# Kernel tuning notes

Hardware: AMD Instinct MI355X
Metric: run time of the kernel (lower is better)

Reference implementation:

```python
import jax, jax.numpy as jnp
import numpy as np

B, S, D, H = 2, 2048, 1024, 16
HD = D // H                 # head_dim = 64
BLOCK = 16                  # _DEFAULT_BLOCK_SIZE
NB = S // BLOCK             # max_blocks_per_seq = 128
WINDOW = 512
NEG = jnp.float32(-1e30)


def setup_inputs() -> dict:
    key = jax.random.key(0)
    ks = jax.random.split(key, 5)
    x = jax.random.normal(ks[0], (B, S, D), jnp.float32)
    scale = D ** -0.5
    wq = jax.random.normal(ks[1], (D, D), jnp.float32) * scale
    wk = jax.random.normal(ks[2], (D, D), jnp.float32) * scale
    wv = jax.random.normal(ks[3], (D, D), jnp.float32) * scale
    wo = jax.random.normal(ks[4], (D, D), jnp.float32) * scale
    # sequential paged layout (matches the module's synthesized-cache fallback)
    block_tables = jnp.arange(B * NB, dtype=jnp.int32).reshape(B, NB)
    slot_mapping = jnp.arange(B * S, dtype=jnp.int32)
    context_lens = jnp.full((B,), S, dtype=jnp.int32)
    return {"x": x, "wq": wq, "wk": wk, "wv": wv, "wo": wo,
            "block_tables": block_tables, "slot_mapping": slot_mapping,
            "context_lens": context_lens, "window_size": WINDOW}


def reference(x, wq, wk, wv, wo, block_tables, slot_mapping, context_lens, window_size):
    b, s, d = x.shape
    # Q/K/V projections (nn.Linear, bias=False: y = x @ W^T)
    q = (x @ wq.T).reshape(b, s, H, HD)
    k = (x @ wk.T).reshape(b, s, H, HD)
    v = (x @ wv.T).reshape(b, s, H, HD)

    # ---- memopt_C.write_cache: scatter K/V into the physical slot pool ----
    num_slots = b * s
    key_cache = jnp.zeros((num_slots, H, HD), x.dtype).at[slot_mapping].set(k.reshape(-1, H, HD))
    value_cache = jnp.zeros((num_slots, H, HD), x.dtype).at[slot_mapping].set(v.reshape(-1, H, HD))

    # ---- dynamic_sparse_attention: read KV through block_tables ----
    t = jnp.arange(s)
    # physical slot of logical token t of sequence b: block_tables[b, t//BLOCK]*BLOCK + t%BLOCK
    slots = block_tables[:, t // BLOCK].astype(jnp.int32) * BLOCK + (t % BLOCK)[None, :].astype(jnp.int32)  # [B,S]
    kc = key_cache[slots]    # [B,S,H,HD]
    vc = value_cache[slots]  # [B,S,H,HD]

    scores = jnp.einsum('bqhd,bkhd->bhqk', q, kc) * (HD ** -0.5)  # [B,H,S,S]
    qpos = t[:, None]
    kpos = t[None, :]
    # causal + window-limited visibility (window_size tokens of history)
    vis = (kpos <= qpos) & (qpos - kpos < window_size)            # [S,S]
    ctx = t[None, :] < context_lens[:, None]                       # [B,S]
    mask = vis[None, None, :, :] & ctx[:, None, None, :]
    scores = jnp.where(mask, scores, NEG)
    attn = jax.nn.softmax(scores, axis=-1)
    out = jnp.einsum('bhqk,bkhd->bqhd', attn, vc).reshape(b, s, d)
    return out @ wo.T
```

## Files before the change

### kernel.cpp

```cpp
#include <hip/hip_runtime.h>

typedef __attribute__((ext_vector_type(4))) float  f32x4;
typedef __attribute__((ext_vector_type(8))) short  bf16x8;

typedef __attribute__((address_space(3))) void lds_void_t;
typedef __attribute__((address_space(1))) void g_void_t;

#define S_LEN  2048
#define DMODEL 1024
#define NHEAD  16
#define HDIM   64
#define NBLK   128
#define BATCH  2
#define KT     64
#define VP     72

__device__ __forceinline__ short f2bf(float f) {
  union { float f; unsigned u; } v; v.f = f;
  unsigned r = v.u + 0x7fffu + ((v.u >> 16) & 1u);
  return (short)(r >> 16);
}

__global__ __launch_bounds__(256) void cvt_all_kernel(
    const float* __restrict__ x,  const float* __restrict__ wq,
    const float* __restrict__ wk, const float* __restrict__ wv,
    const float* __restrict__ wo,
    short* __restrict__ xb,  short* __restrict__ wqb,
    short* __restrict__ wkb, short* __restrict__ wvb,
    short* __restrict__ wob) {
  const long i = ((long)blockIdx.x * 256 + threadIdx.x) * 8;
  const float* s; short* d; long off;
  if (i < 4194304L)      { s = x;  d = xb;  off = i; }
  else if (i < 5242880L) { s = wq; d = wqb; off = i - 4194304L; }
  else if (i < 6291456L) { s = wk; d = wkb; off = i - 5242880L; }
  else if (i < 7340032L) { s = wv; d = wvb; off = i - 6291456L; }
  else                   { s = wo; d = wob; off = i - 7340032L; }
  f32x4 a = *(const f32x4*)(s + off);
  f32x4 b = *(const f32x4*)(s + off + 4);
  bf16x8 o;
  o[0]=f2bf(a[0]); o[1]=f2bf(a[1]); o[2]=f2bf(a[2]); o[3]=f2bf(a[3]);
  o[4]=f2bf(b[0]); o[5]=f2bf(b[1]); o[6]=f2bf(b[2]); o[7]=f2bf(b[3]);
  *(bf16x8*)(d + off) = o;
}

__global__ __launch_bounds__(512, 2) void gemm8_kernel(
    const short* __restrict__ A,
    const short* __restrict__ W0, const short* __restrict__ W1, const short* __restrict__ W2,
    const int* __restrict__ slot_map,
    short* __restrict__ qbuf, short* __restrict__ kcache, short* __restrict__ vcache)
{
  extern __shared__ short smem[];

  const int bid0 = (int)blockIdx.y * 16 + (int)blockIdx.x;
  const int bid  = (bid0 & 7) * 32 + (bid0 >> 3);
  const int m0 = (bid & 15) * 256;
  const int n0 = (bid >> 4) * 192;
  const short* Ag = A + (size_t)m0 * DMODEL;

  const int tid  = threadIdx.x;
  const int wave = tid >> 6, lane = tid & 63;
  const int l15 = lane & 15, lg = lane >> 4;
  const int wr = wave >> 2, wc = wave & 3;
  const int swz = l15 & 7;

  f32x4 acc[8][3];
#pragma unroll
  for (int m = 0; m < 8; m++)
#pragma unroll
    for (int n = 0; n < 3; n++) acc[m][n] = (f32x4)0.f;

#define STG_A(BUFI, K0, P) {                                                               \
    const int g_ = (P) * 512 + tid;                                                        \
    const int r_ = g_ >> 3;                                                                \
    const int cs_ = (g_ & 7) ^ (r_ & 7);                                                   \
    __builtin_amdgcn_global_load_lds((g_void_t*)(Ag + (size_t)r_ * DMODEL + (K0) + cs_ * 8), \
        (lds_void_t*)(smem + (BUFI) * 16384 + ((P) * 512 + wave * 64) * 8), 16, 0, 0); }

#define STG_B(BUFI, K0, P) {                                                               \
    const int g_ = (P) * 512 + tid;                                                        \
    const int r_ = g_ >> 3;                                                                \
    const int grow = n0 + r_;                                                              \
    const short* wb = (grow < 1024) ? W0 : (grow < 2048) ? W1 : W2;                        \
    const int cs_ = (g_ & 7) ^ (r_ & 7);                                                   \
    __builtin_amdgcn_global_load_lds((g_void_t*)(wb + (size_t)(grow & 1023) * DMODEL + (K0) + cs_ * 8), \
        (lds_void_t*)(smem + 49152 + (BUFI) * 12288 + ((P) * 512 + wave * 64) * 8), 16, 0, 0); }

#define BAR() do { asm volatile("" ::: "memory");                \
    __builtin_amdgcn_s_barrier();                                \
    asm volatile("" ::: "memory"); } while (0)

#define LGKM0() asm volatile("s_waitcnt lgkmcnt(0)" ::: "memory")

#define RD_B(BUF)                                                                          \
    _Pragma("unroll") for (int nt = 0; nt < 3; ++nt) {                                     \
      const int row = wc * 48 + nt * 16 + l15;                                             \
      _Pragma("unroll") for (int ks = 0; ks < 2; ++ks)                                     \
        bfr[nt][ks] = *(const bf16x8*)((BUF) + row * 64 + (((ks * 4 + lg) ^ swz) << 3)); }

#define RD_A2(BUF, MQ)                                                                     \
    _Pragma("unroll") for (int mi = 0; mi < 2; ++mi) {                                     \
      const int row = wr * 128 + ((MQ) * 2 + mi) * 16 + l15;                               \
      _Pragma("unroll") for (int ks = 0; ks < 2; ++ks)                                     \
        af[mi][ks] = *(const bf16x8*)((BUF) + row * 64 + (((ks * 4 + lg) ^ swz) << 3)); }

#define MMA2(MQ)                                                                           \
    __builtin_amdgcn_s_setprio(1);                                                         \
    _Pragma("unroll") for (int mi = 0; mi < 2; ++mi)                                       \
    _Pragma("unroll") for (int nt = 0; nt < 3; ++nt)                                       \
    _Pragma("unroll") for (int ks = 0; ks < 2; ++ks)                                       \
      acc[(MQ) * 2 + mi][nt] = __builtin_amdgcn_mfma_f32_16x16x32_bf16(                    \
          af[mi][ks], bfr[nt][ks], acc[(MQ) * 2 + mi][nt], 0, 0, 0);                       \
    __builtin_amdgcn_s_setprio(0);

  const int NT = DMODEL / 64;

  STG_A(0, 0, 0); STG_A(0, 0, 1); STG_A(0, 0, 2); STG_A(0, 0, 3);
  STG_B(0, 0, 0); STG_B(0, 0, 1); STG_B(0, 0, 2);
  STG_A(1, 64, 0); STG_A(1, 64, 1); STG_A(1, 64, 2); STG_A(1, 64, 3);
  asm volatile("s_waitcnt vmcnt(4)" ::: "memory");
  BAR();

  for (int t = 0; t < NT; ++t) {
    const short* Ab = smem + (t % 3) * 16384;
    const short* Bb = smem + 49152 + (t & 1) * 12288;
    const int bB = (t + 1) & 1;
    const int bA = (t + 2) % 3;
    const int k1 = (t + 1) * 64;
    const int k2 = (t + 2) * 64;
    const bool sB = (t + 1 < NT);
    const bool sA = (t + 2 < NT);

    bf16x8 af[2][2], bfr[3][2];

    RD_B(Bb);
    RD_A2(Ab, 0);
    if (sB) { STG_B(bB, k1, 0); }
    if (sA) { STG_A(bA, k2, 0); }
    BAR(); LGKM0();
    MMA2(0);

    RD_A2(Ab, 1);
    if (sB) { STG_B(bB, k1, 1); }
    if (sA) { STG_A(bA, k2, 1); }
    BAR(); LGKM0();
    MMA2(1);

    RD_A2(Ab, 2);
    if (sB) { STG_B(bB, k1, 2); }
    if (sA) { STG_A(bA, k2, 2); }
    BAR(); LGKM0();
    MMA2(2);

    RD_A2(Ab, 3);
    if (sA) { STG_A(bA, k2, 3); }
    BAR(); LGKM0();
    MMA2(3);
    if (t < NT - 2)       { asm volatile("s_waitcnt vmcnt(2)" ::: "memory"); BAR(); }
    else if (t == NT - 2) { asm volatile("s_waitcnt vmcnt(0)" ::: "memory"); BAR(); }
  }
#undef STG_A
#undef STG_B
#undef BAR
#undef LGKM0
#undef RD_B
#undef RD_A2
#undef MMA2

#pragma unroll
  for (int mf = 0; mf < 8; ++mf) {
    const int rowb = m0 + wr * 128 + mf * 16 + lg * 4;
#pragma unroll
    for (int r4 = 0; r4 < 4; ++r4) {
      const int row = rowb + r4;
      const int slot = slot_map[row];
#pragma unroll
      for (int nt = 0; nt < 3; ++nt) {
        const int col = n0 + wc * 48 + nt * 16 + l15;
        const short bv = f2bf(acc[mf][nt][r4]);
        if (col < DMODEL)
          qbuf[(size_t)row * DMODEL + col] = bv;
        else if (col < 2 * DMODEL)
          kcache[(size_t)slot * DMODEL + (col - DMODEL)] = bv;
        else
          vcache[(size_t)slot * DMODEL + (col - 2 * DMODEL)] = bv;
      }
    }
  }
}

__global__ __launch_bounds__(256, 2) void gemm1_kernel(
    const short* __restrict__ A, const short* __restrict__ W,
    float* __restrict__ outf)
{
  extern __shared__ short smem1[];

  const int bid0 = (int)blockIdx.y * 32 + (int)blockIdx.x;
  const int bid  = (bid0 & 7) * 32 + (bid0 >> 3);
  const int m0 = (bid & 31) * 128;
  const int n0 = (bid >> 5) * 128;
  const short* Ag = A + (size_t)m0 * DMODEL;
  const short* Bg = W + (size_t)n0 * DMODEL;

  const int tid = threadIdx.x;
  const int wave = tid >> 6, lane = tid & 63;
  const int l15 = lane & 15, lg = lane >> 4;
  const int wr = wave >> 1, wc = wave & 1;
  const int swz = l15 & 7;

  short* const As0 = smem1;
  short* const Bs0 = smem1 + 8192;
  short* const As1 = smem1 + 16384;
  short* const Bs1 = smem1 + 24576;

  f32x4 acc[4][4];
#pragma unroll
  for (int m = 0; m < 4; m++)
#pragma unroll
    for (int n = 0; n < 4; n++) acc[m][n] = (f32x4)0.f;

#define STG1(LA, LB, K0) {                                                                 \
    _Pragma("unroll") for (int p = 0; p < 4; ++p) {                                        \
      const int u = p * 256 + tid; const int r = u >> 3; const int cs = (u & 7) ^ (r & 7); \
      __builtin_amdgcn_global_load_lds((g_void_t*)(Ag + (size_t)r * DMODEL + (K0) + cs * 8), \
          (lds_void_t*)((LA) + (p * 256 + wave * 64) * 8), 16, 0, 0); }                    \
    _Pragma("unroll") for (int p = 0; p < 4; ++p) {                                        \
      const int u = p * 256 + tid; const int r = u >> 3; const int cs = (u & 7) ^ (r & 7); \
      __builtin_amdgcn_global_load_lds((g_void_t*)(Bg + (size_t)r * DMODEL + (K0) + cs * 8), \
          (lds_void_t*)((LB) + (p * 256 + wave * 64) * 8), 16, 0, 0); } }

  STG1(As0, Bs0, 0);
  asm volatile("s_waitcnt vmcnt(0)" ::: "memory");
  __builtin_amdgcn_s_barrier();
  asm volatile("" ::: "memory");

  for (int t = 0; t < 16; ++t) {
    const int cur = t & 1;
    short* const Ac = cur ? As1 : As0;
    short* const Bc = cur ? Bs1 : Bs0;
    short* const An = cur ? As0 : As1;
    short* const Bn = cur ? Bs0 : Bs1;
    if (t + 1 < 16) {
      STG1(An, Bn, (t + 1) * 64);
      asm volatile("s_waitcnt vmcnt(8)" ::: "memory");
    } else {
      asm volatile("s_waitcnt vmcnt(0)" ::: "memory");
    }
    asm volatile("" ::: "memory");
    __builtin_amdgcn_s_barrier();
    asm volatile("" ::: "memory");

    bf16x8 af[4][2], bfr[4][2];
#pragma unroll
    for (int m4 = 0; m4 < 4; ++m4) {
      const int row = wr * 64 + m4 * 16 + l15;
#pragma unroll
      for (int ks = 0; ks < 2; ++ks)
        af[m4][ks] = *(const bf16x8*)(Ac + row * 64 + (((ks * 4 + lg) ^ swz) << 3));
    }
#pragma unroll
    for (int n4 = 0; n4 < 4; ++n4) {
      const int row = wc * 64 + n4 * 16 + l15;
#pragma unroll
      for (int ks = 0; ks < 2; ++ks)
        bfr[n4][ks] = *(const bf16x8*)(Bc + row * 64 + (((ks * 4 + lg) ^ swz) << 3));
    }
    __builtin_amdgcn_s_setprio(1);
#pragma unroll
    for (int m4 = 0; m4 < 4; ++m4)
#pragma unroll
      for (int n4 = 0; n4 < 4; ++n4)
#pragma unroll
        for (int ks = 0; ks < 2; ++ks)
          acc[m4][n4] = __builtin_amdgcn_mfma_f32_16x16x32_bf16(af[m4][ks], bfr[n4][ks], acc[m4][n4], 0, 0, 0);
    __builtin_amdgcn_s_setprio(0);

    asm volatile("" ::: "memory");
    __builtin_amdgcn_s_barrier();
    asm volatile("" ::: "memory");
  }
#undef STG1

#pragma unroll
  for (int m4 = 0; m4 < 4; ++m4) {
    const int rowb = m0 + wr * 64 + m4 * 16 + lg * 4;
#pragma unroll
    for (int n4 = 0; n4 < 4; ++n4) {
      const int col = n0 + wc * 64 + n4 * 16 + l15;
#pragma unroll
      for (int r4 = 0; r4 < 4; ++r4)
        outf[(size_t)(rowb + r4) * DMODEL + col] = acc[m4][n4][r4];
    }
  }
}

__global__ __launch_bounds__(512, 4) void attn_kernel(
    const short* __restrict__ qbuf,
    const short* __restrict__ kcache, const short* __restrict__ vcache,
    const int* __restrict__ block_tables, const int* __restrict__ context_lens,
    const int* __restrict__ window_size,
    short* __restrict__ attn_out)
{
  __shared__ short Ks[KT * 64];
  __shared__ short Vt[HDIM * VP];
  __shared__ short Pb[8 * 16 * VP];

  const int b = blockIdx.z, h = blockIdx.y;
  const int bx = (b & 1) ? ((int)gridDim.x - 1 - (int)blockIdx.x) : (int)blockIdx.x;
  const int q0 = bx * 128;
  const int ctx = context_lens[b];
  const int ws  = window_size[0];
  const int* bt = block_tables + b * NBLK;

  const int tid  = threadIdx.x;
  const int wave = tid >> 6, lane = tid & 63;
  const int l15 = lane & 15, lg = lane >> 4;
  const int qw = q0 + wave * 16;

  const short* qp = qbuf + ((size_t)(b * S_LEN + qw + l15)) * DMODEL + h * HDIM;
  const bf16x8 qf0 = *(const bf16x8*)(qp + lg * 8);
  const bf16x8 qf1 = *(const bf16x8*)(qp + 32 + lg * 8);

  f32x4 oacc[4];
  float lrow[4];
#pragma unroll
  for (int i = 0; i < 4; i++) { oacc[i] = (f32x4)0.f; lrow[i] = 0.f; }

  int kstart = q0 - ws + 1; if (kstart < 0) kstart = 0; kstart &= ~(KT - 1);
  int kend = q0 + 128; if (kend > ctx) kend = ctx;

  const int kr = tid >> 3;
  const int dc = (tid & 7) << 3;
  const float rscale = 0.125f;
  const float FM = 12.f;
  short* pw = Pb + wave * (16 * VP);
  const int swz = (l15 & 7) << 4;

  bf16x8 kreg = (bf16x8)0, vreg = (bf16x8)0;
  {
    const int key = kstart + kr;
    if (key < ctx) {
      const int slot = bt[key >> 4] * 16 + (key & 15);
      kreg = *(const bf16x8*)(kcache + (size_t)slot * DMODEL + h * HDIM + dc);
      vreg = *(const bf16x8*)(vcache + (size_t)slot * DMODEL + h * HDIM + dc);
    }
  }

  for (int kt = kstart; kt < kend; kt += KT) {
    __syncthreads();
    *(bf16x8*)((char*)Ks + kr * 128 + ((dc * 2) ^ ((kr & 7) << 4))) = kreg;
    const int vcol = (kr + dc) & 63;
#pragma unroll
    for (int j = 0; j < 8; j++) Vt[(dc + j) * VP + vcol] = vreg[j];
    kreg = (bf16x8)0; vreg = (bf16x8)0;
    if (kt + KT < kend) {
      const int key = kt + KT + kr;
      if (key < ctx) {
        const int slot = bt[key >> 4] * 16 + (key & 15);
        kreg = *(const bf16x8*)(kcache + (size_t)slot * DMODEL + h * HDIM + dc);
        vreg = *(const bf16x8*)(vcache + (size_t)slot * DMODEL + h * HDIM + dc);
      }
    }
    __syncthreads();

    if ((kt > qw + 15) || (kt + (KT - 1) <= qw - ws)) continue;

    f32x4 sacc[4];
#pragma unroll
    for (int cg = 0; cg < 4; cg++) sacc[cg] = (f32x4)0.f;
#pragma unroll
    for (int cg = 0; cg < 4; cg++) {
      const char* kp = (const char*)Ks + (cg * 16 + l15) * 128;
      const bf16x8 k0 = *(const bf16x8*)(kp + ((lg * 16) ^ swz));
      const bf16x8 k1 = *(const bf16x8*)(kp + ((64 + lg * 16) ^ swz));
      sacc[cg] = __builtin_amdgcn_mfma_f32_16x16x32_bf16(qf0, k0, sacc[cg], 0, 0, 0);
      sacc[cg] = __builtin_amdgcn_mfma_f32_16x16x32_bf16(qf1, k1, sacc[cg], 0, 0, 0);
    }

    const bool fullvis = (kt + (KT - 1) <= qw) && (qw + 15 - kt < ws) && (kt + (KT - 1) < ctx);

    if (fullvis) {
#pragma unroll
      for (int r = 0; r < 4; r++) {
        const float e0 = __expf(sacc[0][r] * rscale - FM);
        const float e1 = __expf(sacc[1][r] * rscale - FM);
        const float e2 = __expf(sacc[2][r] * rscale - FM);
        const float e3 = __expf(sacc[3][r] * rscale - FM);
        lrow[r] += (e0 + e1) + (e2 + e3);
        short* pr = pw + (lg * 4 + r) * VP + l15;
        pr[0]  = f2bf(e0); pr[16] = f2bf(e1);
        pr[32] = f2bf(e2); pr[48] = f2bf(e3);
      }
    } else {
#pragma unroll
      for (int r = 0; r < 4; r++) {
        const int qrow = qw + lg * 4 + r;
        const int key0 = kt + l15;
        const bool ok0 = (key0      <= qrow) && (qrow - key0      < ws) && (key0      < ctx);
        const bool ok1 = (key0 + 16 <= qrow) && (qrow - key0 - 16 < ws) && (key0 + 16 < ctx);
        const bool ok2 = (key0 + 32 <= qrow) && (qrow - key0 - 32 < ws) && (key0 + 32 < ctx);
        const bool ok3 = (key0 + 48 <= qrow) && (qrow - key0 - 48 < ws) && (key0 + 48 < ctx);
        const float e0 = ok0 ? __expf(sacc[0][r] * rscale - FM) : 0.f;
        const float e1 = ok1 ? __expf(sacc[1][r] * rscale - FM) : 0.f;
        const float e2 = ok2 ? __expf(sacc[2][r] * rscale - FM) : 0.f;
        const float e3 = ok3 ? __expf(sacc[3][r] * rscale - FM) : 0.f;
        lrow[r] += (e0 + e1) + (e2 + e3);
        short* pr = pw + (lg * 4 + r) * VP + l15;
        pr[0]  = f2bf(e0); pr[16] = f2bf(e1);
        pr[32] = f2bf(e2); pr[48] = f2bf(e3);
      }
    }

    asm volatile("s_waitcnt lgkmcnt(0)" ::: "memory");

#pragma unroll
    for (int kk = 0; kk < 2; kk++) {
      const bf16x8 pa = *(const bf16x8*)(pw + l15 * VP + kk * 32 + lg * 8);
#pragma unroll
      for (int dn = 0; dn < 4; dn++) {
        const int vrow = dn * 16 + l15;
        const int roff = (kk * 32 + lg * 8 + (vrow & ~7)) & 63;
        const bf16x8 vb = *(const bf16x8*)(Vt + vrow * VP + roff);
        oacc[dn] = __builtin_amdgcn_mfma_f32_16x16x32_bf16(pa, vb, oacc[dn], 0, 0, 0);
      }
    }
  }

#pragma unroll
  for (int r = 0; r < 4; r++) {
    float ls = lrow[r];
    ls += __shfl_xor(ls, 1); ls += __shfl_xor(ls, 2);
    ls += __shfl_xor(ls, 4); ls += __shfl_xor(ls, 8);
    const float inv = 1.f / fmaxf(ls, 1e-30f);
    const int row = qw + lg * 4 + r;
    short* op = attn_out + ((size_t)(b * S_LEN + row)) * DMODEL + h * HDIM;
#pragma unroll
    for (int dn = 0; dn < 4; dn++)
      op[dn * 16 + l15] = f2bf(oacc[dn][r] * inv);
  }
}

extern "C" void kernel_launch(void* const* d_in, const int* in_sizes, int n_in,
                              void* d_out, int out_size, void* d_ws, size_t ws_size,
                              hipStream_t stream) {
  const float* x  = (const float*)d_in[0];
  const float* wq = (const float*)d_in[1];
  const float* wk = (const float*)d_in[2];
  const float* wv = (const float*)d_in[3];
  const float* wo = (const float*)d_in[4];
  const int* block_tables = (const int*)d_in[5];
  const int* slot_mapping = (const int*)d_in[6];
  const int* context_lens = (const int*)d_in[7];
  const int* window_size  = (const int*)d_in[8];
  float* out = (float*)d_out;

  char* ws = (char*)d_ws;
  short* xb     = (short*)(ws + (size_t)( 0 << 20));
  short* wqb    = (short*)(ws + (size_t)( 8 << 20));
  short* wkb    = (short*)(ws + (size_t)(10 << 20));
  short* wvb    = (short*)(ws + (size_t)(12 << 20));
  short* wob    = (short*)(ws + (size_t)(14 << 20));
  short* qbuf   = (short*)(ws + (size_t)(16 << 20));
  short* kcache = (short*)(ws + (size_t)(24 << 20));
  short* vcache = (short*)(ws + (size_t)(32 << 20));
  short* abuf   = (short*)(ws + (size_t)(40 << 20));

  static bool ginit = [] {
    hipFuncSetAttribute(reinterpret_cast<const void*>(&gemm8_kernel),
                        hipFuncAttributeMaxDynamicSharedMemorySize, 147456);
    hipFuncSetAttribute(reinterpret_cast<const void*>(&gemm1_kernel),
                        hipFuncAttributeMaxDynamicSharedMemorySize, 65536);
    return true;
  }();
  (void)ginit;

  cvt_all_kernel<<<4096, 256, 0, stream>>>(x, wq, wk, wv, wo, xb, wqb, wkb, wvb, wob);

  gemm8_kernel<<<dim3(16, 16), 512, 147456, stream>>>(xb, wqb, wkb, wvb, slot_mapping,
                                                      qbuf, kcache, vcache);

  attn_kernel<<<dim3(S_LEN / 128, NHEAD, BATCH), 512, 0, stream>>>(
      qbuf, kcache, vcache, block_tables, context_lens, window_size, abuf);

  gemm1_kernel<<<dim3(32, 8), 256, 65536, stream>>>(abuf, wob, out);
}
```

Baseline: 90.00 us.

## Process 32 query rows per wave in attention to reuse K/V tiles

```diff
diff --git a/kernel.cpp b/kernel.cpp
--- a/kernel.cpp
+++ b/kernel.cpp
@@ -293,7 +293,7 @@
   }
 }
 
-__global__ __launch_bounds__(512, 4) void attn_kernel(
+__global__ __launch_bounds__(512, 2) void attn_kernel(
     const short* __restrict__ qbuf,
     const short* __restrict__ kcache, const short* __restrict__ vcache,
     const int* __restrict__ block_tables, const int* __restrict__ context_lens,
@@ -302,11 +302,11 @@
 {
   __shared__ short Ks[KT * 64];
   __shared__ short Vt[HDIM * VP];
-  __shared__ short Pb[8 * 16 * VP];
+  __shared__ short Pb[8 * 32 * VP];
 
   const int b = blockIdx.z, h = blockIdx.y;
   const int bx = (b & 1) ? ((int)gridDim.x - 1 - (int)blockIdx.x) : (int)blockIdx.x;
-  const int q0 = bx * 128;
+  const int q0 = bx * 256;
   const int ctx = context_lens[b];
   const int ws  = window_size[0];
   const int* bt = block_tables + b * NBLK;
@@ -314,25 +314,31 @@
   const int tid  = threadIdx.x;
   const int wave = tid >> 6, lane = tid & 63;
   const int l15 = lane & 15, lg = lane >> 4;
-  const int qw = q0 + wave * 16;
-
-  const short* qp = qbuf + ((size_t)(b * S_LEN + qw + l15)) * DMODEL + h * HDIM;
-  const bf16x8 qf0 = *(const bf16x8*)(qp + lg * 8);
-  const bf16x8 qf1 = *(const bf16x8*)(qp + 32 + lg * 8);
-
-  f32x4 oacc[4];
-  float lrow[4];
-#pragma unroll
-  for (int i = 0; i < 4; i++) { oacc[i] = (f32x4)0.f; lrow[i] = 0.f; }
+  const int qw = q0 + wave * 32;
+
+  bf16x8 qf[2][2];
+#pragma unroll
+  for (int rg = 0; rg < 2; rg++) {
+    const short* qp = qbuf + ((size_t)(b * S_LEN + qw + rg * 16 + l15)) * DMODEL + h * HDIM;
+    qf[rg][0] = *(const bf16x8*)(qp + lg * 8);
+    qf[rg][1] = *(const bf16x8*)(qp + 32 + lg * 8);
+  }
+
+  f32x4 oacc[2][4];
+  float lrow[2][4];
+#pragma unroll
+  for (int rg = 0; rg < 2; rg++)
+#pragma unroll
+    for (int i = 0; i < 4; i++) { oacc[rg][i] = (f32x4)0.f; lrow[rg][i] = 0.f; }
 
   int kstart = q0 - ws + 1; if (kstart < 0) kstart = 0; kstart &= ~(KT - 1);
-  int kend = q0 + 128; if (kend > ctx) kend = ctx;
+  int kend = q0 + 256; if (kend > ctx) kend = ctx;
 
   const int kr = tid >> 3;
   const int dc = (tid & 7) << 3;
   const float rscale = 0.125f;
   const float FM = 12.f;
-  short* pw = Pb + wave * (16 * VP);
+  short* pw = Pb + wave * (32 * VP);
   const int swz = (l15 & 7) << 4;
 
   bf16x8 kreg = (bf16x8)0, vreg = (bf16x8)0;
@@ -362,80 +368,90 @@
     }
     __syncthreads();
 
-    if ((kt > qw + 15) || (kt + (KT - 1) <= qw - ws)) continue;
-
-    f32x4 sacc[4];
-#pragma unroll
-    for (int cg = 0; cg < 4; cg++) sacc[cg] = (f32x4)0.f;
-#pragma unroll
-    for (int cg = 0; cg < 4; cg++) {
-      const char* kp = (const char*)Ks + (cg * 16 + l15) * 128;
-      const bf16x8 k0 = *(const bf16x8*)(kp + ((lg * 16) ^ swz));
-      const bf16x8 k1 = *(const bf16x8*)(kp + ((64 + lg * 16) ^ swz));
-      sacc[cg] = __builtin_amdgcn_mfma_f32_16x16x32_bf16(qf0, k0, sacc[cg], 0, 0, 0);
-      sacc[cg] = __builtin_amdgcn_mfma_f32_16x16x32_bf16(qf1, k1, sacc[cg], 0, 0, 0);
-    }
-
-    const bool fullvis = (kt + (KT - 1) <= qw) && (qw + 15 - kt < ws) && (kt + (KT - 1) < ctx);
-
-    if (fullvis) {
-#pragma unroll
-      for (int r = 0; r < 4; r++) {
-        const float e0 = __expf(sacc[0][r] * rscale - FM);
-        const float e1 = __expf(sacc[1][r] * rscale - FM);
-        const float e2 = __expf(sacc[2][r] * rscale - FM);
-        const float e3 = __expf(sacc[3][r] * rscale - FM);
-        lrow[r] += (e0 + e1) + (e2 + e3);
-        short* pr = pw + (lg * 4 + r) * VP + l15;
-        pr[0]  = f2bf(e0); pr[16] = f2bf(e1);
-        pr[32] = f2bf(e2); pr[48] = f2bf(e3);
+    if ((kt > qw + 31) || (kt + (KT - 1) <= qw - ws)) continue;
+
+#pragma unroll
+    for (int rg = 0; rg < 2; rg++) {
+      f32x4 sacc[4];
+#pragma unroll
+      for (int cg = 0; cg < 4; cg++) sacc[cg] = (f32x4)0.f;
+#pragma unroll
+      for (int cg = 0; cg < 4; cg++) {
+        const char* kp = (const char*)Ks + (cg * 16 + l15) * 128;
+        const bf16x8 k0 = *(const bf16x8*)(kp + ((lg * 16) ^ swz));
+        const bf16x8 k1 = *(const bf16x8*)(kp + ((64 + lg * 16) ^ swz));
+        sacc[cg] = __builtin_amdgcn_mfma_f32_16x16x32_bf16(qf[rg][0], k0, sacc[cg], 0, 0, 0);
+        sacc[cg] = __builtin_amdgcn_mfma_f32_16x16x32_bf16(qf[rg][1], k1, sacc[cg], 0, 0, 0);
       }
-    } else {
-#pragma unroll
-      for (int r = 0; r < 4; r++) {
-        const int qrow = qw + lg * 4 + r;
-        const int key0 = kt + l15;
-        const bool ok0 = (key0      <= qrow) && (qrow - key0      < ws) && (key0      < ctx);
-        const bool ok1 = (key0 + 16 <= qrow) && (qrow - key0 - 16 < ws) && (key0 + 16 < ctx);
-        const bool ok2 = (key0 + 32 <= qrow) && (qrow - key0 - 32 < ws) && (key0 + 32 < ctx);
-        const bool ok3 = (key0 + 48 <= qrow) && (qrow - key0 - 48 < ws) && (key0 + 48 < ctx);
-        const float e0 = ok0 ? __expf(sacc[0][r] * rscale - FM) : 0.f;
-        const float e1 = ok1 ? __expf(sacc[1][r] * rscale - FM) : 0.f;
-        const float e2 = ok2 ? __expf(sacc[2][r] * rscale - FM) : 0.f;
-        const float e3 = ok3 ? __expf(sacc[3][r] * rscale - FM) : 0.f;
-        lrow[r] += (e0 + e1) + (e2 + e3);
-        short* pr = pw + (lg * 4 + r) * VP + l15;
-        pr[0]  = f2bf(e0); pr[16] = f2bf(e1);
-        pr[32] = f2bf(e2); pr[48] = f2bf(e3);
+
+      const int qb = qw + rg * 16;
+      const bool fullvis = (kt + (KT - 1) <= qb) && (qb + 15 - kt < ws) && (kt + (KT - 1) < ctx);
+
+      if (fullvis) {
+#pragma unroll
+        for (int r = 0; r < 4; r++) {
+          const float e0 = __expf(sacc[0][r] * rscale - FM);
+          const float e1 = __expf(sacc[1][r] * rscale - FM);
+          const float e2 = __expf(sacc[2][r] * rscale - FM);
+          const float e3 = __expf(sacc[3][r] * rscale - FM);
+          lrow[rg][r] += (e0 + e1) + (e2 + e3);
+          short* pr = pw + (rg * 16 + lg * 4 + r) * VP + l15;
+          pr[0]  = f2bf(e0); pr[16] = f2bf(e1);
+          pr[32] = f2bf(e2); pr[48] = f2bf(e3);
+        }
+      } else {
+#pragma unroll
+        for (int r = 0; r < 4; r++) {
+          const int qrow = qb + lg * 4 + r;
+          const int key0 = kt + l15;
+          const bool ok0 = (key0      <= qrow) && (qrow - key0      < ws) && (key0      < ctx);
+          const bool ok1 = (key0 + 16 <= qrow) && (qrow - key0 - 16 < ws) && (key0 + 16 < ctx);
+          const bool ok2 = (key0 + 32 <= qrow) && (qrow - key0 - 32 < ws) && (key0 + 32 < ctx);
+          const bool ok3 = (key0 + 48 <= qrow) && (qrow - key0 - 48 < ws) && (key0 + 48 < ctx);
+          const float e0 = ok0 ? __expf(sacc[0][r] * rscale - FM) : 0.f;
+          const float e1 = ok1 ? __expf(sacc[1][r] * rscale - FM) : 0.f;
+          const float e2 = ok2 ? __expf(sacc[2][r] * rscale - FM) : 0.f;
+          const float e3 = ok3 ? __expf(sacc[3][r] * rscale - FM) : 0.f;
+          lrow[rg][r] += (e0 + e1) + (e2 + e3);
+          short* pr = pw + (rg * 16 + lg * 4 + r) * VP + l15;
+          pr[0]  = f2bf(e0); pr[16] = f2bf(e1);
+          pr[32] = f2bf(e2); pr[48] = f2bf(e3);
+        }
       }
     }
 
     asm volatile("s_waitcnt lgkmcnt(0)" ::: "memory");
 
 #pragma unroll
-    for (int kk = 0; kk < 2; kk++) {
-      const bf16x8 pa = *(const bf16x8*)(pw + l15 * VP + kk * 32 + lg * 8);
-#pragma unroll
-      for (int dn = 0; dn < 4; dn++) {
-        const int vrow = dn * 16 + l15;
-        const int roff = (kk * 32 + lg * 8 + (vrow & ~7)) & 63;
-        const bf16x8 vb = *(const bf16x8*)(Vt + vrow * VP + roff);
-        oacc[dn] = __builtin_amdgcn_mfma_f32_16x16x32_bf16(pa, vb, oacc[dn], 0, 0, 0);
+    for (int rg = 0; rg < 2; rg++) {
+#pragma unroll
+      for (int kk = 0; kk < 2; kk++) {
+        const bf16x8 pa = *(const bf16x8*)(pw + (rg * 16 + l15) * VP + kk * 32 + lg * 8);
+#pragma unroll
+        for (int dn = 0; dn < 4; dn++) {
+          const int vrow = dn * 16 + l15;
+          const int roff = (kk * 32 + lg * 8 + (vrow & ~7)) & 63;
+          const bf16x8 vb = *(const bf16x8*)(Vt + vrow * VP + roff);
+          oacc[rg][dn] = __builtin_amdgcn_mfma_f32_16x16x32_bf16(pa, vb, oacc[rg][dn], 0, 0, 0);
+        }
       }
     }
   }
 
 #pragma unroll
-  for (int r = 0; r < 4; r++) {
-    float ls = lrow[r];
-    ls += __shfl_xor(ls, 1); ls += __shfl_xor(ls, 2);
-    ls += __shfl_xor(ls, 4); ls += __shfl_xor(ls, 8);
-    const float inv = 1.f / fmaxf(ls, 1e-30f);
-    const int row = qw + lg * 4 + r;
-    short* op = attn_out + ((size_t)(b * S_LEN + row)) * DMODEL + h * HDIM;
-#pragma unroll
-    for (int dn = 0; dn < 4; dn++)
-      op[dn * 16 + l15] = f2bf(oacc[dn][r] * inv);
+  for (int rg = 0; rg < 2; rg++) {
+#pragma unroll
+    for (int r = 0; r < 4; r++) {
+      float ls = lrow[rg][r];
+      ls += __shfl_xor(ls, 1); ls += __shfl_xor(ls, 2);
+      ls += __shfl_xor(ls, 4); ls += __shfl_xor(ls, 8);
+      const float inv = 1.f / fmaxf(ls, 1e-30f);
+      const int row = qw + rg * 16 + lg * 4 + r;
+      short* op = attn_out + ((size_t)(b * S_LEN + row)) * DMODEL + h * HDIM;
+#pragma unroll
+      for (int dn = 0; dn < 4; dn++)
+        op[dn * 16 + l15] = f2bf(oacc[rg][dn][r] * inv);
+    }
   }
 }
 
@@ -478,7 +494,7 @@
   gemm8_kernel<<<dim3(16, 16), 512, 147456, stream>>>(xb, wqb, wkb, wvb, slot_mapping,
                                                       qbuf, kcache, vcache);
 
-  attn_kernel<<<dim3(S_LEN / 128, NHEAD, BATCH), 512, 0, stream>>>(
+  attn_kernel<<<dim3(S_LEN / 256, NHEAD, BATCH), 512, 0, stream>>>(
       qbuf, kcache, vcache, block_tables, context_lens, window_size, abuf);
 
   gemm1_kernel<<<dim3(32, 8), 256, 65536, stream>>>(abuf, wob, out);
```

After: 95.68 us. 1.06x slower.
